# Performance work log

Hardware: AMD Instinct MI355X
Metric: run time of the kernel (lower is better)

## Reference

```python
import jax, jax.numpy as jnp
import numpy as np

N_NODES = 100000
N_EDGES = 3200000
D_IN = 256
D_OUT = 256


def setup_inputs() -> dict:
    key = jax.random.key(0)
    k1, k2, k3, k4, k5, k6 = jax.random.split(key, 6)
    x = jax.random.normal(k1, (N_NODES, D_IN), dtype=jnp.float32)
    edge_row = jax.random.randint(k2, (N_EDGES,), 0, N_NODES, dtype=jnp.int32)
    edge_col = jax.random.randint(k3, (N_EDGES,), 0, N_NODES, dtype=jnp.int32)
    edge_val = jax.random.uniform(k4, (N_EDGES,), dtype=jnp.float32)
    # nn.Linear params (PyTorch stores weight as [out, in]; we apply x @ W.T + b)
    bound = 1.0 / np.sqrt(D_IN)
    W = jax.random.uniform(k5, (D_OUT, D_IN), minval=-bound, maxval=bound, dtype=jnp.float32)
    b = jax.random.uniform(k6, (D_OUT,), minval=-bound, maxval=bound, dtype=jnp.float32)
    return {"x": x, "edge_row": edge_row, "edge_col": edge_col,
            "edge_val": edge_val, "W": W, "b": b}


def reference(x, edge_row, edge_col, edge_val, W, b):
    # SpMM: agg[i] = sum over edges e with row[e]==i of val[e] * x[col[e]]
    messages = edge_val[:, None] * x[edge_col]          # [E, D_in]
    agg = jax.ops.segment_sum(messages, edge_row, num_segments=N_NODES)  # [N, D_in]
    # Dense linear: agg @ W.T + b
    return jnp.einsum('nd,od->no', agg, W) + b
```

## Files before the change

kernel.cpp:

```cpp
#include <hip/hip_runtime.h>

#define THREADS 256
#define P2T 512
#define P1B 1024
#define CVTXB 1536

typedef __attribute__((ext_vector_type(8))) short short8;
typedef __attribute__((ext_vector_type(4))) float f32x4;

__device__ __forceinline__ unsigned short f2bf(float f) {
    unsigned u = __builtin_bit_cast(unsigned, f);
    return (unsigned short)((u + 0x7FFFu + ((u >> 16) & 1u)) >> 16);
}
__device__ __forceinline__ float bf2f_lo(unsigned u) { return __builtin_bit_cast(float, u << 16); }
__device__ __forceinline__ float bf2f_hi(unsigned u) { return __builtin_bit_cast(float, u & 0xFFFF0000u); }

__global__ void fusedA_kernel(const int* __restrict__ row, const int* __restrict__ col,
                              const float* __restrict__ val, int* __restrict__ gcur,
                              uint2* __restrict__ estage,
                              const float* __restrict__ W, unsigned short* __restrict__ WbP,
                              const float4* __restrict__ x, uint4* __restrict__ xb,
                              int n_edges, int nbkt, int capS, int n8) {
    int b = blockIdx.x, tid = threadIdx.x;
    if (b < P1B) {
        __shared__ int h[512];
        __shared__ int curl[512];
        int g = b & 7;
        int E0 = (int)((long long)b * n_edges / P1B);
        int E1 = (int)((long long)(b + 1) * n_edges / P1B);
        for (int i = tid; i < 512; i += THREADS) h[i] = 0;
        __syncthreads();
        for (int e = E0 + tid; e < E1; e += THREADS)
            atomicAdd(&h[row[e] >> 8], 1);
        __syncthreads();
        for (int bk = tid; bk < nbkt; bk += THREADS) {
            int c = h[bk];
            curl[bk] = (bk * 8 + g) * capS + (c ? atomicAdd(&gcur[bk * 8 + g], c) : 0);
        }
        __syncthreads();
        for (int e = E0 + tid; e < E1; e += THREADS) {
            int r = row[e];
            int bk = r >> 8;
            int pos = atomicAdd(&curl[bk], 1);
            if (pos < (bk * 8 + g + 1) * capS)
                estage[pos] = make_uint2(((unsigned)(r & 255) << 24) | (unsigned)col[e],
                                         (unsigned)__float_as_int(val[e]));
        }
    } else if (b < P1B + 32) {
        int f = (b - P1B) * THREADS + tid;
        int l = f & 63, nt = (f >> 6) & 15, k0i = f >> 10;
        int r = nt * 16 + (l & 15);
        int koff = k0i * 32 + 8 * (l >> 4);
        const float4* s = reinterpret_cast<const float4*>(W + r * 256 + koff);
        float4 a = s[0], bb = s[1];
        uint4 o;
        o.x = (unsigned)f2bf(a.x) | ((unsigned)f2bf(a.y) << 16);
        o.y = (unsigned)f2bf(a.z) | ((unsigned)f2bf(a.w) << 16);
        o.z = (unsigned)f2bf(bb.x) | ((unsigned)f2bf(bb.y) << 16);
        o.w = (unsigned)f2bf(bb.z) | ((unsigned)f2bf(bb.w) << 16);
        reinterpret_cast<uint4*>(WbP)[f] = o;
    } else {
        int stride = CVTXB * THREADS;
        for (int i = (b - P1B - 32) * THREADS + tid; i < n8; i += stride) {
            float4 a = x[2 * i], bb = x[2 * i + 1];
            uint4 o;
            o.x = (unsigned)f2bf(a.x) | ((unsigned)f2bf(a.y) << 16);
            o.y = (unsigned)f2bf(a.z) | ((unsigned)f2bf(a.w) << 16);
            o.z = (unsigned)f2bf(bb.x) | ((unsigned)f2bf(bb.y) << 16);
            o.w = (unsigned)f2bf(bb.z) | ((unsigned)f2bf(bb.w) << 16);
            reinterpret_cast<uint4*>(xb)[i] = o;
        }
    }
}

__global__ void p2_sort(const uint2* __restrict__ estage, const int* __restrict__ gcur,
                        int2* __restrict__ pr, int* __restrict__ offs,
                        int capS, int n_nodes, int nbkt) {
    __shared__ int red[P2T];
    __shared__ int h[256];
    __shared__ int curh[256];
    __shared__ int wsum[4];
    __shared__ int scnt[8];
    int b = blockIdx.x, tid = threadIdx.x;

    int lim = b * 8;
    int partial = 0;
    for (int j = tid; j < lim; j += P2T) {
        int c = gcur[j];
        partial += c > capS ? capS : c;
    }
    red[tid] = partial;
    __syncthreads();
    #pragma unroll
    for (int s = P2T / 2; s > 0; s >>= 1) {
        if (tid < s) red[tid] += red[tid + s];
        __syncthreads();
    }
    int gb = red[0];
    if (tid < 8) {
        int c = gcur[b * 8 + tid];
        scnt[tid] = c > capS ? capS : c;
    }
    if (tid < 256) h[tid] = 0;
    __syncthreads();

    #pragma unroll
    for (int g = 0; g < 8; ++g) {
        int cnt = scnt[g];
        int base = (b * 8 + g) * capS;
        for (int i = tid; i < cnt; i += P2T)
            atomicAdd(&h[estage[base + i].x >> 24], 1);
    }
    __syncthreads();
    if (tid < 256) {
        int v = h[tid];
        int lane = tid & 63, w = tid >> 6;
        int incl = v;
        #pragma unroll
        for (int off = 1; off < 64; off <<= 1) {
            int t = __shfl_up(incl, off, 64);
            if (lane >= off) incl += t;
        }
        if (lane == 63) wsum[w] = incl;
        __syncthreads();
        int wo = 0;
        for (int i = 0; i < w; ++i) wo += wsum[i];
        int excl = wo + incl - v;
        int node = b * 256 + tid;
        if (node < n_nodes) offs[node] = gb + excl;
        curh[tid] = gb + excl;
    } else {
        __syncthreads();
    }
    if (b == nbkt - 1 && tid == 0) {
        int t = 0;
        #pragma unroll
        for (int g = 0; g < 8; ++g) t += scnt[g];
        offs[n_nodes] = gb + t;
    }
    __syncthreads();
    #pragma unroll
    for (int g = 0; g < 8; ++g) {
        int cnt = scnt[g];
        int base = (b * 8 + g) * capS;
        for (int i = tid; i < cnt; i += P2T) {
            uint2 p = estage[base + i];
            int q = atomicAdd(&curh[(int)(p.x >> 24)], 1);
            pr[q] = make_int2((int)(p.x & 0x00FFFFFFu), (int)p.y);
        }
    }
}

template<int OUT_BF16>
__global__ void spmm_bf16_kernel(const uint2* __restrict__ xb, const int* __restrict__ offs,
                                 const int2* __restrict__ pr, void* __restrict__ outp,
                                 int b0, int b1, int nnodes) {
    int g = blockIdx.x & 7;
    int inst = blockIdx.x >> 3;
    int bkt = b0 + g + 8 * (inst >> 6);
    if (bkt >= b1) return;
    int wid = bkt * 256 + (inst & 63) * 4 + (threadIdx.x >> 6);
    int lane = threadIdx.x & 63;
    if (wid >= nnodes) return;
    int s = offs[wid], e = offs[wid + 1];
    float a0 = 0.f, a1 = 0.f, a2 = 0.f, a3 = 0.f;
    int i = s;
    if (i < e && (i & 1)) {
        int2 p = pr[i];
        uint2 xv = xb[(size_t)p.x * 64 + lane];
        float v = __int_as_float(p.y);
        a0 = fmaf(v, bf2f_lo(xv.x), a0); a1 = fmaf(v, bf2f_hi(xv.x), a1);
        a2 = fmaf(v, bf2f_lo(xv.y), a2); a3 = fmaf(v, bf2f_hi(xv.y), a3);
        ++i;
    }
    for (; i + 8 <= e; i += 8) {
        int4 pa = *reinterpret_cast<const int4*>(pr + i);
        int4 pb = *reinterpret_cast<const int4*>(pr + i + 2);
        int4 pc = *reinterpret_cast<const int4*>(pr + i + 4);
        int4 pd = *reinterpret_cast<const int4*>(pr + i + 6);
        uint2 x0 = xb[(size_t)pa.x * 64 + lane];
        uint2 x1 = xb[(size_t)pa.z * 64 + lane];
        uint2 x2 = xb[(size_t)pb.x * 64 + lane];
        uint2 x3 = xb[(size_t)pb.z * 64 + lane];
        uint2 x4_ = xb[(size_t)pc.x * 64 + lane];
        uint2 x5 = xb[(size_t)pc.z * 64 + lane];
        uint2 x6 = xb[(size_t)pd.x * 64 + lane];
        uint2 x7 = xb[(size_t)pd.z * 64 + lane];
        float v0 = __int_as_float(pa.y), v1 = __int_as_float(pa.w);
        float v2 = __int_as_float(pb.y), v3 = __int_as_float(pb.w);
        float v4 = __int_as_float(pc.y), v5 = __int_as_float(pc.w);
        float v6 = __int_as_float(pd.y), v7 = __int_as_float(pd.w);
        a0 = fmaf(v0, bf2f_lo(x0.x), a0); a1 = fmaf(v0, bf2f_hi(x0.x), a1);
        a2 = fmaf(v0, bf2f_lo(x0.y), a2); a3 = fmaf(v0, bf2f_hi(x0.y), a3);
        a0 = fmaf(v1, bf2f_lo(x1.x), a0); a1 = fmaf(v1, bf2f_hi(x1.x), a1);
        a2 = fmaf(v1, bf2f_lo(x1.y), a2); a3 = fmaf(v1, bf2f_hi(x1.y), a3);
        a0 = fmaf(v2, bf2f_lo(x2.x), a0); a1 = fmaf(v2, bf2f_hi(x2.x), a1);
        a2 = fmaf(v2, bf2f_lo(x2.y), a2); a3 = fmaf(v2, bf2f_hi(x2.y), a3);
        a0 = fmaf(v3, bf2f_lo(x3.x), a0); a1 = fmaf(v3, bf2f_hi(x3.x), a1);
        a2 = fmaf(v3, bf2f_lo(x3.y), a2); a3 = fmaf(v3, bf2f_hi(x3.y), a3);
        a0 = fmaf(v4, bf2f_lo(x4_.x), a0); a1 = fmaf(v4, bf2f_hi(x4_.x), a1);
        a2 = fmaf(v4, bf2f_lo(x4_.y), a2); a3 = fmaf(v4, bf2f_hi(x4_.y), a3);
        a0 = fmaf(v5, bf2f_lo(x5.x), a0); a1 = fmaf(v5, bf2f_hi(x5.x), a1);
        a2 = fmaf(v5, bf2f_lo(x5.y), a2); a3 = fmaf(v5, bf2f_hi(x5.y), a3);
        a0 = fmaf(v6, bf2f_lo(x6.x), a0); a1 = fmaf(v6, bf2f_hi(x6.x), a1);
        a2 = fmaf(v6, bf2f_lo(x6.y), a2); a3 = fmaf(v6, bf2f_hi(x6.y), a3);
        a0 = fmaf(v7, bf2f_lo(x7.x), a0); a1 = fmaf(v7, bf2f_hi(x7.x), a1);
        a2 = fmaf(v7, bf2f_lo(x7.y), a2); a3 = fmaf(v7, bf2f_hi(x7.y), a3);
    }
    for (; i + 2 <= e; i += 2) {
        int4 pa = *reinterpret_cast<const int4*>(pr + i);
        uint2 x0 = xb[(size_t)pa.x * 64 + lane];
        uint2 x1 = xb[(size_t)pa.z * 64 + lane];
        float v0 = __int_as_float(pa.y), v1 = __int_as_float(pa.w);
        a0 = fmaf(v0, bf2f_lo(x0.x), a0); a1 = fmaf(v0, bf2f_hi(x0.x), a1);
        a2 = fmaf(v0, bf2f_lo(x0.y), a2); a3 = fmaf(v0, bf2f_hi(x0.y), a3);
        a0 = fmaf(v1, bf2f_lo(x1.x), a0); a1 = fmaf(v1, bf2f_hi(x1.x), a1);
        a2 = fmaf(v1, bf2f_lo(x1.y), a2); a3 = fmaf(v1, bf2f_hi(x1.y), a3);
    }
    for (; i < e; ++i) {
        int2 p = pr[i];
        uint2 xv = xb[(size_t)p.x * 64 + lane];
        float v = __int_as_float(p.y);
        a0 = fmaf(v, bf2f_lo(xv.x), a0); a1 = fmaf(v, bf2f_hi(xv.x), a1);
        a2 = fmaf(v, bf2f_lo(xv.y), a2); a3 = fmaf(v, bf2f_hi(xv.y), a3);
    }
    if (OUT_BF16) {
        ushort4 o;
        o.x = f2bf(a0); o.y = f2bf(a1); o.z = f2bf(a2); o.w = f2bf(a3);
        *reinterpret_cast<ushort4*>((unsigned short*)outp + (size_t)wid * 256 + 4 * lane) = o;
    } else {
        ((float4*)outp)[(size_t)wid * 64 + lane] = make_float4(a0, a1, a2, a3);
    }
}

__global__ void spmm_f32_kernel(const float4* __restrict__ x4, const int* __restrict__ offs,
                                const int2* __restrict__ pr, float4* __restrict__ out4,
                                int nnodes) {
    int wid = (blockIdx.x * blockDim.x + threadIdx.x) >> 6;
    int lane = threadIdx.x & 63;
    if (wid >= nnodes) return;
    int s = offs[wid], e = offs[wid + 1];
    float4 acc = make_float4(0.f, 0.f, 0.f, 0.f);
    for (int i = s; i < e; ++i) {
        int2 p = pr[i];
        float4 xv = x4[(size_t)p.x * 64 + lane];
        float v = __int_as_float(p.y);
        acc.x = fmaf(v, xv.x, acc.x); acc.y = fmaf(v, xv.y, acc.y);
        acc.z = fmaf(v, xv.z, acc.z); acc.w = fmaf(v, xv.w, acc.w);
    }
    out4[(size_t)wid * 64 + lane] = acc;
}

__launch_bounds__(256)
__global__ void gemm_direct3_kernel(const unsigned short* __restrict__ aggb,
                                    const unsigned short* __restrict__ WbP,
                                    const float* __restrict__ bias,
                                    float* __restrict__ out, int n) {
    int tid = threadIdx.x, lane = tid & 63, w = tid >> 6;
    int row0 = blockIdx.x * 128 + w * 32;
    int lr = lane & 15, lg = lane >> 4;
    const unsigned short* arow0 = aggb + (size_t)(row0 + lr) * 256 + lg * 8;
    const unsigned short* arow1 = arow0 + 16 * 256;
    short8 af0[8], af1[8];
    #pragma unroll
    for (int k = 0; k < 8; ++k) {
        af0[k] = *reinterpret_cast<const short8*>(arow0 + k * 32);
        af1[k] = *reinterpret_cast<const short8*>(arow1 + k * 32);
    }
    #pragma unroll
    for (int half = 0; half < 2; ++half) {
        f32x4 acc0[8], acc1[8];
        #pragma unroll
        for (int nt = 0; nt < 8; ++nt) {
            acc0[nt] = (f32x4){0.f, 0.f, 0.f, 0.f};
            acc1[nt] = (f32x4){0.f, 0.f, 0.f, 0.f};
        }
        #pragma unroll
        for (int k = 0; k < 8; ++k) {
            #pragma unroll
            for (int nt = 0; nt < 8; ++nt) {
                short8 bf_ = *reinterpret_cast<const short8*>(
                    &WbP[(size_t)((k * 16 + half * 8 + nt) * 64 + lane) * 8]);
                acc0[nt] = __builtin_amdgcn_mfma_f32_16x16x32_bf16(af0[k], bf_, acc0[nt], 0, 0, 0);
                acc1[nt] = __builtin_amdgcn_mfma_f32_16x16x32_bf16(af1[k], bf_, acc1[nt], 0, 0, 0);
            }
        }
        #pragma unroll
        for (int nt = 0; nt < 8; ++nt) {
            int gc = half * 128 + nt * 16 + lr;
            float bv = bias[gc];
            #pragma unroll
            for (int q = 0; q < 4; ++q) {
                int gr0 = row0 + lg * 4 + q;
                int gr1 = gr0 + 16;
                if (gr0 < n) out[(size_t)gr0 * 256 + gc] = acc0[nt][q] + bv;
                if (gr1 < n) out[(size_t)gr1 * 256 + gc] = acc1[nt][q] + bv;
            }
        }
    }
}


__global__ void zero_kernel(int* __restrict__ p, int n) {
    int i = blockIdx.x * blockDim.x + threadIdx.x;
    if (i < n) p[i] = 0;
}

__global__ void hist_part_kernel(const int* __restrict__ row, int* __restrict__ cnt,
                                 int n_edges, int n_nodes) {
    int g = blockIdx.x & 7;
    int inst = blockIdx.x >> 3;
    int ninst = gridDim.x >> 3;
    int lo = (int)(((long long)g * n_nodes) >> 3);
    int hi = (int)(((long long)(g + 1) * n_nodes) >> 3);
    int e0 = (int)(((long long)inst * n_edges) / ninst);
    int e1 = (int)(((long long)(inst + 1) * n_edges) / ninst);
    for (int e = e0 + threadIdx.x; e < e1; e += THREADS) {
        int r = row[e];
        if (r >= lo && r < hi) atomicAdd(&cnt[r], 1);
    }
}

__global__ void place_part_kernel(const int* __restrict__ row, const int* __restrict__ col,
                                  const float* __restrict__ val, int* __restrict__ cur,
                                  int2* __restrict__ pr, int n_edges, int n_nodes) {
    int g = blockIdx.x & 7;
    int inst = blockIdx.x >> 3;
    int ninst = gridDim.x >> 3;
    int lo = (int)(((long long)g * n_nodes) >> 3);
    int hi = (int)(((long long)(g + 1) * n_nodes) >> 3);
    int e0 = (int)(((long long)inst * n_edges) / ninst);
    int e1 = (int)(((long long)(inst + 1) * n_edges) / ninst);
    for (int e = e0 + threadIdx.x; e < e1; e += THREADS) {
        int r = row[e];
        if (r >= lo && r < hi) {
            int p = atomicAdd(&cur[r], 1);
            pr[p] = make_int2(col[e], __float_as_int(val[e]));
        }
    }
}

__global__ void scan1_kernel(const int* __restrict__ cnt, int* __restrict__ offs,
                             int* __restrict__ bsum, int n) {
    int tid = threadIdx.x;
    int base = blockIdx.x * 1024 + tid * 4;
    int v0 = 0, v1 = 0, v2 = 0, v3 = 0;
    if (base + 3 < n) {
        int4 v = *reinterpret_cast<const int4*>(cnt + base);
        v0 = v.x; v1 = v.y; v2 = v.z; v3 = v.w;
    } else {
        if (base + 0 < n) v0 = cnt[base + 0];
        if (base + 1 < n) v1 = cnt[base + 1];
        if (base + 2 < n) v2 = cnt[base + 2];
    }
    int ts = v0 + v1 + v2 + v3;
    int lane = tid & 63;
    int incl = ts;
    #pragma unroll
    for (int off = 1; off < 64; off <<= 1) {
        int t = __shfl_up(incl, off, 64);
        if (lane >= off) incl += t;
    }
    __shared__ int wsum[4];
    int w = tid >> 6;
    if (lane == 63) wsum[w] = incl;
    __syncthreads();
    int wo = 0;
    for (int i = 0; i < w; ++i) wo += wsum[i];
    int excl = wo + incl - ts;
    if (base + 0 < n) offs[base + 0] = excl;
    if (base + 1 < n) offs[base + 1] = excl + v0;
    if (base + 2 < n) offs[base + 2] = excl + v0 + v1;
    if (base + 3 < n) offs[base + 3] = excl + v0 + v1 + v2;
    if (tid == THREADS - 1) bsum[blockIdx.x] = wo + incl;
}

__global__ void scan2_kernel(int* __restrict__ bsum, int nb) {
    int tid = threadIdx.x;
    int base = tid * 4;
    int v0 = 0, v1 = 0, v2 = 0, v3 = 0;
    if (base + 0 < nb) v0 = bsum[base + 0];
    if (base + 1 < nb) v1 = bsum[base + 1];
    if (base + 2 < nb) v2 = bsum[base + 2];
    if (base + 3 < nb) v3 = bsum[base + 3];
    int ts = v0 + v1 + v2 + v3;
    int lane = tid & 63;
    int incl = ts;
    #pragma unroll
    for (int off = 1; off < 64; off <<= 1) {
        int t = __shfl_up(incl, off, 64);
        if (lane >= off) incl += t;
    }
    __shared__ int wsum[4];
    int w = tid >> 6;
    if (lane == 63) wsum[w] = incl;
    __syncthreads();
    int wo = 0;
    for (int i = 0; i < w; ++i) wo += wsum[i];
    int excl = wo + incl - ts;
    if (base + 0 < nb) bsum[base + 0] = excl;
    if (base + 1 < nb) bsum[base + 1] = excl + v0;
    if (base + 2 < nb) bsum[base + 2] = excl + v0 + v1;
    if (base + 3 < nb) bsum[base + 3] = excl + v0 + v1 + v2;
    if (tid == THREADS - 1) bsum[nb] = wo + incl;
}

__global__ void scan3_kernel(int* __restrict__ offs, const int* __restrict__ bsum,
                             int* __restrict__ cur, int n) {
    int i = blockIdx.x * blockDim.x + threadIdx.x;
    if (i < n) {
        int v = offs[i] + bsum[i >> 10];
        offs[i] = v;
        cur[i] = v;
    }
    if (i == 0) offs[n] = bsum[(n + 1023) >> 10];
}

__global__ void cvt_bf16_kernel(const float4* __restrict__ in, uint4* __restrict__ out, int n8) {
    int i = blockIdx.x * blockDim.x + threadIdx.x;
    if (i >= n8) return;
    float4 a = in[2 * i], b = in[2 * i + 1];
    uint4 o;
    o.x = (unsigned)f2bf(a.x) | ((unsigned)f2bf(a.y) << 16);
    o.y = (unsigned)f2bf(a.z) | ((unsigned)f2bf(a.w) << 16);
    o.z = (unsigned)f2bf(b.x) | ((unsigned)f2bf(b.y) << 16);
    o.w = (unsigned)f2bf(b.z) | ((unsigned)f2bf(b.w) << 16);
    out[i] = o;
}

__launch_bounds__(256, 2)
__global__ void gemm_mfma_kernel(float* __restrict__ out, const unsigned short* __restrict__ Wb,
                                 const float* __restrict__ bias, int nrows) {
    __shared__ unsigned short As[64][264];
    __shared__ unsigned short Ws[256][40];
    int tid = threadIdx.x;
    int rowBase = blockIdx.x * 64;

    const float4* o4 = reinterpret_cast<const float4*>(out);
    for (int it = tid; it < 64 * 64; it += 256) {
        int r = it >> 6, c = it & 63;
        float4 v = make_float4(0.f, 0.f, 0.f, 0.f);
        int gr = rowBase + r;
        if (gr < nrows) v = o4[(size_t)gr * 64 + c];
        ushort4 w;
        w.x = f2bf(v.x); w.y = f2bf(v.y); w.z = f2bf(v.z); w.w = f2bf(v.w);
        *reinterpret_cast<ushort4*>(&As[r][c * 4]) = w;
    }

    int w = tid >> 6, lane = tid & 63;
    int lr = lane & 15, lg = lane >> 4;
    f32x4 acc[16];
    #pragma unroll
    for (int nt = 0; nt < 16; ++nt) acc[nt] = (f32x4){0.f, 0.f, 0.f, 0.f};

    for (int k0 = 0; k0 < 256; k0 += 32) {
        __syncthreads();
        for (int it = tid; it < 1024; it += 256) {
            int r = it >> 2, c = it & 3;
            uint4 v = *reinterpret_cast<const uint4*>(Wb + (size_t)r * 256 + k0 + c * 8);
            *reinterpret_cast<uint4*>(&Ws[r][c * 8]) = v;
        }
        __syncthreads();
        short8 af = *reinterpret_cast<const short8*>(&As[w * 16 + lr][k0 + 8 * lg]);
        #pragma unroll
        for (int nt = 0; nt < 16; ++nt) {
            short8 bf_ = *reinterpret_cast<const short8*>(&Ws[nt * 16 + lr][8 * lg]);
            acc[nt] = __builtin_amdgcn_mfma_f32_16x16x32_bf16(af, bf_, acc[nt], 0, 0, 0);
        }
    }

    #pragma unroll
    for (int nt = 0; nt < 16; ++nt) {
        int gc = nt * 16 + lr;
        float bv = bias[gc];
        #pragma unroll
        for (int q = 0; q < 4; ++q) {
            int gr = rowBase + w * 16 + lg * 4 + q;
            if (gr < nrows) out[(size_t)gr * 256 + gc] = acc[nt][q] + bv;
        }
    }
}


extern "C" void kernel_launch(void* const* d_in, const int* in_sizes, int n_in,
                              void* d_out, int out_size, void* d_ws, size_t ws_size,
                              hipStream_t stream) {
    const float* x     = (const float*)d_in[0];
    const int*   erow  = (const int*)d_in[1];
    const int*   ecol  = (const int*)d_in[2];
    const float* evalv = (const float*)d_in[3];
    const float* W     = (const float*)d_in[4];
    const float* bias  = (const float*)d_in[5];
    float* out = (float*)d_out;

    int n_nodes = in_sizes[0] / 256;
    int n_edges = in_sizes[1];

    int nbkt = (n_nodes + 255) >> 8;
    int avg8 = n_edges / (8 * (nbkt > 0 ? nbkt : 1)) + 1;
    int capS = avg8 + avg8 / 8 + 512;

    size_t A = (size_t)((n_nodes + 63) & ~63) + 64;
    int* offs  = (int*)d_ws;
    int* gcur  = offs + A;
    unsigned short* WbP = (unsigned short*)(gcur + 4096);
    int2* pr = (int2*)(WbP + 65536);
    int* after_pr = (int*)(pr + n_edges);

    size_t est_ints  = (size_t)nbkt * 8 * capS * 2;
    size_t aggb_ints = (size_t)n_nodes * 128 + 32768;
    size_t xb_ints   = (size_t)n_nodes * 128;
    size_t alias_ints = est_ints > aggb_ints ? est_ints : aggb_ints;
    size_t head_ints = (size_t)(after_pr - (int*)d_ws);
    size_t need_new = (head_ints + alias_ints + xb_ints) * 4;
    bool new_ok = (nbkt <= 512) && (nbkt >= 1) && (n_nodes <= (1 << 24)) && ws_size >= need_new;

    if (new_ok) {
        uint2* estage = (uint2*)after_pr;
        unsigned short* aggb = (unsigned short*)after_pr;
        unsigned short* xb = (unsigned short*)(after_pr + alias_ints);

        hipMemsetAsync(gcur, 0, 4096 * sizeof(int), stream);
        int n8 = n_nodes * 32;
        fusedA_kernel<<<P1B + 32 + CVTXB, THREADS, 0, stream>>>(
            erow, ecol, evalv, gcur, estage, W, WbP, (const float4*)x, (uint4*)xb,
            n_edges, nbkt, capS, n8);
        p2_sort<<<nbkt, P2T, 0, stream>>>(estage, gcur, pr, offs, capS, n_nodes, nbkt);

        int b0 = 0;
        for (int sseg = 1; sseg <= 2; ++sseg) {
            int b1 = (sseg == 2) ? nbkt : ((nbkt / 2) & ~7);
            if (b1 <= b0) continue;
            int grid = 8 * (((b1 - b0) + 7) / 8) * 64;
            spmm_bf16_kernel<1><<<grid, THREADS, 0, stream>>>(
                (const uint2*)xb, offs, pr, aggb, b0, b1, n_nodes);
            b0 = b1;
        }
        int gb = (n_nodes + 127) / 128;
        gemm_direct3_kernel<<<gb, THREADS, 0, stream>>>(aggb, WbP, bias, out, n_nodes);
    } else {
        int nb = (n_nodes + 1023) >> 10;
        size_t Af = (size_t)((n_nodes + 63) & ~63);
        int* cnt   = (int*)d_ws;
        int* offsf = cnt + Af;
        int* cur   = offsf + Af;
        int* bsum  = cur + Af;
        int* wbase = bsum + (((size_t)nb + 64) & ~63ull);
        unsigned short* Wbf = (unsigned short*)wbase;
        int2* prf  = (int2*)(Wbf + 65536);
        int* aft   = (int*)(prf + n_edges);
        unsigned short* xbf = (unsigned short*)aft;
        size_t need_old = (size_t)((char*)(xbf + (size_t)n_nodes * 256) - (char*)d_ws);
        bool told = ws_size >= need_old;

        zero_kernel<<<(n_nodes + THREADS - 1) / THREADS, THREADS, 0, stream>>>(cnt, n_nodes);
        hist_part_kernel<<<2048, THREADS, 0, stream>>>(erow, cnt, n_edges, n_nodes);
        scan1_kernel<<<nb, THREADS, 0, stream>>>(cnt, offsf, bsum, n_nodes);
        scan2_kernel<<<1, THREADS, 0, stream>>>(bsum, nb);
        scan3_kernel<<<(n_nodes + THREADS - 1) / THREADS, THREADS, 0, stream>>>(offsf, bsum, cur, n_nodes);
        place_part_kernel<<<2048, THREADS, 0, stream>>>(erow, ecol, evalv, cur, prf, n_edges, n_nodes);
        cvt_bf16_kernel<<<32, THREADS, 0, stream>>>((const float4*)W, (uint4*)Wbf, 65536 / 8);

        int gb = (n_nodes + 63) / 64;
        if (told) {
            int n8 = n_nodes * 32;
            cvt_bf16_kernel<<<(n8 + THREADS - 1) / THREADS, THREADS, 0, stream>>>(
                (const float4*)x, (uint4*)xbf, n8);
            int nbf = (n_nodes + 255) / 256;
            int gridf = 8 * ((nbf + 7) / 8) * 64;
            spmm_bf16_kernel<0><<<gridf, THREADS, 0, stream>>>(
                (const uint2*)xbf, offsf, prf, out, 0, nbf, n_nodes);
        } else {
            int spmm_blocks_f = (n_nodes + 3) / 4;
            spmm_f32_kernel<<<spmm_blocks_f, THREADS, 0, stream>>>(
                (const float4*)x, offsf, prf, (float4*)out, n_nodes);
        }
        gemm_mfma_kernel<<<gb, THREADS, 0, stream>>>(out, Wbf, bias, n_nodes);
    }
}
```

Measured before the change: 432.5 us.

## Presort edges per block in LDS before coalesced scatter; split conversion kernel; single SpMM launch

The edge bucketing pass now stages each block's edges in shared memory, ordered by bucket through a scan, and then writes them to the global staging buffer in contiguous runs instead of scattered per-edge stores. The W/x bf16 conversion moves to its own kernel, and the two-segment SpMM launch becomes a single launch. The goal is to cut scattered global write traffic in the presort. The cost is a large shared-memory footprint (about 32KB) that may lower occupancy, and a new edge-count limit on the fast path.

```diff
diff --git a/kernel.cpp b/kernel.cpp
--- a/kernel.cpp
+++ b/kernel.cpp
@@ -3,6 +3,7 @@
 #define THREADS 256
 #define P2T 512
 #define P1B 1024
+#define MAXEPB 3200
 #define CVTXB 1536
 
 typedef __attribute__((ext_vector_type(8))) short short8;
@@ -15,39 +16,79 @@
 __device__ __forceinline__ float bf2f_lo(unsigned u) { return __builtin_bit_cast(float, u << 16); }
 __device__ __forceinline__ float bf2f_hi(unsigned u) { return __builtin_bit_cast(float, u & 0xFFFF0000u); }
 
-__global__ void fusedA_kernel(const int* __restrict__ row, const int* __restrict__ col,
-                              const float* __restrict__ val, int* __restrict__ gcur,
-                              uint2* __restrict__ estage,
-                              const float* __restrict__ W, unsigned short* __restrict__ WbP,
-                              const float4* __restrict__ x, uint4* __restrict__ xb,
-                              int n_edges, int nbkt, int capS, int n8) {
+__global__ __launch_bounds__(THREADS)
+void p1_presort_kernel(const int* __restrict__ row, const int* __restrict__ col,
+                       const float* __restrict__ val, int* __restrict__ gcur,
+                       uint2* __restrict__ estage, int n_edges, int nbkt, int capS) {
+    __shared__ int h[512];
+    __shared__ int base[512];
+    __shared__ int gchunk[512];
+    __shared__ int curl[512];
+    __shared__ int wsum[4];
+    __shared__ uint2 rec[MAXEPB];
+    __shared__ unsigned short rbkt[MAXEPB];
+
     int b = blockIdx.x, tid = threadIdx.x;
-    if (b < P1B) {
-        __shared__ int h[512];
-        __shared__ int curl[512];
-        int g = b & 7;
-        int E0 = (int)((long long)b * n_edges / P1B);
-        int E1 = (int)((long long)(b + 1) * n_edges / P1B);
-        for (int i = tid; i < 512; i += THREADS) h[i] = 0;
-        __syncthreads();
-        for (int e = E0 + tid; e < E1; e += THREADS)
-            atomicAdd(&h[row[e] >> 8], 1);
-        __syncthreads();
-        for (int bk = tid; bk < nbkt; bk += THREADS) {
+    int g = b & 7;
+    int E0 = (int)((long long)b * n_edges / P1B);
+    int E1 = (int)((long long)(b + 1) * n_edges / P1B);
+    int cnt = E1 - E0;
+
+    h[2 * tid] = 0; h[2 * tid + 1] = 0;
+    __syncthreads();
+    for (int e = E0 + tid; e < E1; e += THREADS)
+        atomicAdd(&h[row[e] >> 8], 1);
+    __syncthreads();
+    int v0 = h[2 * tid], v1 = h[2 * tid + 1];
+    int ts = v0 + v1;
+    int lane = tid & 63, w = tid >> 6;
+    int incl = ts;
+    #pragma unroll
+    for (int off = 1; off < 64; off <<= 1) {
+        int t = __shfl_up(incl, off, 64);
+        if (lane >= off) incl += t;
+    }
+    if (lane == 63) wsum[w] = incl;
+    __syncthreads();
+    int wo = 0;
+    for (int i = 0; i < w; ++i) wo += wsum[i];
+    int excl = wo + incl - ts;
+    base[2 * tid] = excl;
+    base[2 * tid + 1] = excl + v0;
+    curl[2 * tid] = excl;
+    curl[2 * tid + 1] = excl + v0;
+    #pragma unroll
+    for (int q = 0; q < 2; ++q) {
+        int bk = 2 * tid + q;
+        if (bk < nbkt) {
             int c = h[bk];
-            curl[bk] = (bk * 8 + g) * capS + (c ? atomicAdd(&gcur[bk * 8 + g], c) : 0);
-        }
-        __syncthreads();
-        for (int e = E0 + tid; e < E1; e += THREADS) {
-            int r = row[e];
-            int bk = r >> 8;
-            int pos = atomicAdd(&curl[bk], 1);
-            if (pos < (bk * 8 + g + 1) * capS)
-                estage[pos] = make_uint2(((unsigned)(r & 255) << 24) | (unsigned)col[e],
-                                         (unsigned)__float_as_int(val[e]));
-        }
-    } else if (b < P1B + 32) {
-        int f = (b - P1B) * THREADS + tid;
+            int ro = c ? atomicAdd(&gcur[bk * 8 + g], c) : 0;
+            gchunk[bk] = (bk * 8 + g) * capS + ro;
+        }
+    }
+    __syncthreads();
+    for (int e = E0 + tid; e < E1; e += THREADS) {
+        int r = row[e];
+        int bk = r >> 8;
+        int pos = atomicAdd(&curl[bk], 1);
+        rec[pos] = make_uint2(((unsigned)(r & 255) << 24) | (unsigned)col[e],
+                              (unsigned)__float_as_int(val[e]));
+        rbkt[pos] = (unsigned short)bk;
+    }
+    __syncthreads();
+    for (int i = tid; i < cnt; i += THREADS) {
+        int bk = rbkt[i];
+        int dst = gchunk[bk] + (i - base[bk]);
+        if (dst < (bk * 8 + g + 1) * capS)
+            estage[dst] = rec[i];
+    }
+}
+
+__global__ void cvtWX_kernel(const float* __restrict__ W, unsigned short* __restrict__ WbP,
+                             const float4* __restrict__ x, uint4* __restrict__ xb, int n8) {
+    int b = blockIdx.x, tid = threadIdx.x;
+    if (b < 32) {
+        int f = b * THREADS + tid;
         int l = f & 63, nt = (f >> 6) & 15, k0i = f >> 10;
         int r = nt * 16 + (l & 15);
         int koff = k0i * 32 + 8 * (l >> 4);
@@ -61,7 +102,7 @@
         reinterpret_cast<uint4*>(WbP)[f] = o;
     } else {
         int stride = CVTXB * THREADS;
-        for (int i = (b - P1B - 32) * THREADS + tid; i < n8; i += stride) {
+        for (int i = (b - 32) * THREADS + tid; i < n8; i += stride) {
             float4 a = x[2 * i], bb = x[2 * i + 1];
             uint4 o;
             o.x = (unsigned)f2bf(a.x) | ((unsigned)f2bf(a.y) << 16);
@@ -513,7 +554,8 @@
     size_t alias_ints = est_ints > aggb_ints ? est_ints : aggb_ints;
     size_t head_ints = (size_t)(after_pr - (int*)d_ws);
     size_t need_new = (head_ints + alias_ints + xb_ints) * 4;
-    bool new_ok = (nbkt <= 512) && (nbkt >= 1) && (n_nodes <= (1 << 24)) && ws_size >= need_new;
+    bool new_ok = (nbkt <= 512) && (nbkt >= 1) && (n_nodes <= (1 << 24)) &&
+                  (n_edges <= P1B * (MAXEPB - 64)) && ws_size >= need_new;
 
     if (new_ok) {
         uint2* estage = (uint2*)after_pr;
@@ -522,20 +564,15 @@
 
         hipMemsetAsync(gcur, 0, 4096 * sizeof(int), stream);
         int n8 = n_nodes * 32;
-        fusedA_kernel<<<P1B + 32 + CVTXB, THREADS, 0, stream>>>(
-            erow, ecol, evalv, gcur, estage, W, WbP, (const float4*)x, (uint4*)xb,
-            n_edges, nbkt, capS, n8);
+        cvtWX_kernel<<<32 + CVTXB, THREADS, 0, stream>>>(
+            W, WbP, (const float4*)x, (uint4*)xb, n8);
+        p1_presort_kernel<<<P1B, THREADS, 0, stream>>>(
+            erow, ecol, evalv, gcur, estage, n_edges, nbkt, capS);
         p2_sort<<<nbkt, P2T, 0, stream>>>(estage, gcur, pr, offs, capS, n_nodes, nbkt);
 
-        int b0 = 0;
-        for (int sseg = 1; sseg <= 2; ++sseg) {
-            int b1 = (sseg == 2) ? nbkt : ((nbkt / 2) & ~7);
-            if (b1 <= b0) continue;
-            int grid = 8 * (((b1 - b0) + 7) / 8) * 64;
-            spmm_bf16_kernel<1><<<grid, THREADS, 0, stream>>>(
-                (const uint2*)xb, offs, pr, aggb, b0, b1, n_nodes);
-            b0 = b1;
-        }
+        int grid = 8 * ((nbkt + 7) / 8) * 64;
+        spmm_bf16_kernel<1><<<grid, THREADS, 0, stream>>>(
+            (const uint2*)xb, offs, pr, aggb, 0, nbkt, n_nodes);
         int gb = (n_nodes + 127) / 128;
         gemm_direct3_kernel<<<gb, THREADS, 0, stream>>>(aggb, WbP, bias, out, n_nodes);
     } else {
```

Result: faster. 422.9 us, median of 2 (-2.2%).
